# Performance work log

Hardware: AMD Instinct MI355X
Metric: run time of the kernel (lower is better)

The kernel has to match this reference:

```python
import jax, jax.numpy as jnp
import numpy as np

B, N, D = 8, 2048, 512

def setup_inputs() -> dict:
    key = jax.random.key(0)
    k1, k2, k3, k4, k5 = jax.random.split(key, 5)
    s = 1.0 / np.sqrt(D)
    return {
        "x": jax.random.normal(k1, (B, N, D), dtype=jnp.float32),
        "w_qkv": jax.random.normal(k2, (D, 3 * D), dtype=jnp.float32) * s,
        "b_qkv": jax.random.normal(k3, (3 * D,), dtype=jnp.float32) * 0.01,
        "w_fc": jax.random.normal(k4, (D, D), dtype=jnp.float32) * s,
        "b_fc": jax.random.normal(k5, (D,), dtype=jnp.float32) * 0.01,
    }

def reference(x, w_qkv, b_qkv, w_fc, b_fc):
    scale = 1.0 / (x.shape[-1] ** 0.5)
    qkv = x @ w_qkv + b_qkv                      # [B, N, 3D]
    q, k, v = jnp.split(qkv, 3, axis=-1)         # each [B, N, D]
    attn = jnp.einsum("bnd,bmd->bnm", q, k) * scale
    attn = jax.nn.softmax(attn, axis=-1)
    out = jnp.einsum("bnm,bmd->bnd", attn, v)
    return out @ w_fc + b_fc + x
```

## Files before the change

### kernel.cpp

```cpp
#include <hip/hip_runtime.h>
#include <stdint.h>

typedef unsigned short u16;
typedef unsigned int u32;
typedef __attribute__((ext_vector_type(8))) short short8;
typedef __attribute__((ext_vector_type(4))) float f32x4;
typedef __attribute__((ext_vector_type(8))) unsigned short u16x8;
typedef __attribute__((ext_vector_type(4))) float float4_t;

__device__ __forceinline__ float b2f(u16 u) { return __uint_as_float(((u32)u) << 16); }
__device__ __forceinline__ u16 f2b(float f) {
  u32 u = __float_as_uint(f);
  u += 0x7fffu + ((u >> 16) & 1u);
  return (u16)(u >> 16);
}

typedef const __attribute__((address_space(1))) void* gas_t;
typedef __attribute__((address_space(3))) void* las_t;
__device__ __forceinline__ void gl_lds16(const void* g, void* l) {
  __builtin_amdgcn_global_load_lds((gas_t)(uintptr_t)g, (las_t)(u32)(uintptr_t)l, 16, 0, 0);
}

__global__ __launch_bounds__(256) void cvt_f2b_kernel(const float* __restrict__ src,
                                                      u16* __restrict__ dst, long n) {
  long i = ((long)blockIdx.x * 256 + threadIdx.x) * 8;
  if (i >= n) return;
  float4_t v0 = *(const float4_t*)(src + i);
  float4_t v1 = *(const float4_t*)(src + i + 4);
  u16x8 o;
#pragma unroll
  for (int j = 0; j < 4; ++j) { o[j] = f2b(v0[j]); o[4 + j] = f2b(v1[j]); }
  *(u16x8*)(dst + i) = o;
}

__global__ __launch_bounds__(256) void tr_cvt(const float* __restrict__ src,
                                              u16* __restrict__ dst, int R, int C) {
  __shared__ float t[32][33];
  const int bx = blockIdx.x * 32;
  const int by = blockIdx.y * 32;
  const int tx = threadIdx.x & 31, ty = threadIdx.x >> 5;
#pragma unroll
  for (int i = 0; i < 32; i += 8)
    t[ty + i][tx] = src[(long)(by + ty + i) * C + bx + tx];
  __syncthreads();
#pragma unroll
  for (int i = 0; i < 32; i += 8)
    dst[(long)(bx + ty + i) * R + by + tx] = f2b(t[tx][ty + i]);
}

__global__ __launch_bounds__(256) void tr_v(const u16* __restrict__ qkv, u16* __restrict__ vt) {
  __shared__ u16 t[32][33];
  const int b = blockIdx.z;
  const int r0 = blockIdx.x * 32;
  const int d0 = blockIdx.y * 32;
  const int tx = threadIdx.x & 31, ty = threadIdx.x >> 5;
#pragma unroll
  for (int i = 0; i < 32; i += 8)
    t[ty + i][tx] = qkv[((long)b * 2048 + r0 + ty + i) * 1536 + 1024 + d0 + tx];
  __syncthreads();
#pragma unroll
  for (int i = 0; i < 32; i += 8)
    vt[((long)b * 512 + d0 + ty + i) * 2048 + r0 + tx] = t[tx][ty + i];
}

template <bool OUT_F32, bool BIAS, bool RES>
__global__ __launch_bounds__(256)
void gemm_bt(const u16* __restrict__ A, const u16* __restrict__ Bt, void* __restrict__ Cv,
             const float* __restrict__ bias, const float* __restrict__ res,
             int K, int lda, int ldb, int ldc,
             long aStride, long bStride, long cStride, float alpha) {
  __shared__ u16 As[2][128 * 32];
  __shared__ u16 Bs[2][128 * 32];
  const int tid = threadIdx.x;
  const int wid = tid >> 6, lane = tid & 63;
  const int wm = (wid >> 1) * 64, wn = (wid & 1) * 64;

  const int gx = gridDim.x, gy = gridDim.y;
  int id = (blockIdx.z * gy + blockIdx.y) * gx + blockIdx.x;
  const int nwg = gx * gy * gridDim.z;
  id = (id & 7) * (nwg >> 3) + (id >> 3);
  const int bxi = id % gx;
  const int t2 = id / gx;
  const int byi = t2 % gy;
  const long z = t2 / gy;

  A += z * aStride;
  Bt += z * bStride;
  const int by = byi * 128;
  const int bx = bxi * 128;

  f32x4 acc[4][4] = {};

  const int srow = wid * 32 + (lane >> 2);
  const int scol_lin = (lane & 3) * 8;
  const int scol_src = (((lane & 3) ^ ((lane >> 3) & 3)) * 8);
  const u16* Ag0 = A + (long)(by + srow) * lda + scol_src;
  const u16* Ag1 = Ag0 + (long)16 * lda;
  const u16* Bg0 = Bt + (long)(bx + srow) * ldb + scol_src;
  const u16* Bg1 = Bg0 + (long)16 * ldb;
  const int sL0 = srow * 32 + scol_lin;
  const int sL1 = sL0 + 16 * 32;
  const int lr = lane & 15, lg = lane >> 4;
  const int swz = ((lr >> 1) & 3) ^ lg;
  const int nK = K >> 5;

  auto stage = [&](int u, int nb) {
    const long ko = (long)u * 32;
    gl_lds16(Ag0 + ko, &As[nb][sL0]);
    gl_lds16(Ag1 + ko, &As[nb][sL1]);
    gl_lds16(Bg0 + ko, &Bs[nb][sL0]);
    gl_lds16(Bg1 + ko, &Bs[nb][sL1]);
  };

  stage(0, 0);

  for (int t = 0; t < nK; ++t) {
    const int cur = t & 1;
    asm volatile("s_waitcnt vmcnt(0)" ::: "memory");
    __builtin_amdgcn_s_barrier();
    __builtin_amdgcn_sched_barrier(0);
    if (t + 1 < nK) stage(t + 1, cur ^ 1);

    short8 a[4], b[4];
#pragma unroll
    for (int i = 0; i < 4; ++i) {
      a[i] = *(const short8*)&As[cur][(wm + i * 16 + lr) * 32 + swz * 8];
      b[i] = *(const short8*)&Bs[cur][(wn + i * 16 + lr) * 32 + swz * 8];
    }
    __builtin_amdgcn_s_setprio(1);
#pragma unroll
    for (int mi = 0; mi < 4; ++mi)
#pragma unroll
      for (int ni = 0; ni < 4; ++ni)
        acc[mi][ni] = __builtin_amdgcn_mfma_f32_16x16x32_bf16(a[mi], b[ni], acc[mi][ni], 0, 0, 0);
    __builtin_amdgcn_s_setprio(0);
  }

  if constexpr (OUT_F32) {
    float* C = (float*)Cv + z * cStride;
#pragma unroll
    for (int mi = 0; mi < 4; ++mi)
#pragma unroll
      for (int ni = 0; ni < 4; ++ni)
#pragma unroll
        for (int j = 0; j < 4; ++j) {
          const long row = by + wm + mi * 16 + lg * 4 + j;
          const int col = bx + wn + ni * 16 + lr;
          float v = acc[mi][ni][j] * alpha;
          if (BIAS) v += bias[col];
          if (RES) v += res[row * (long)ldc + col];
          C[row * (long)ldc + col] = v;
        }
  } else {
    u16* C = (u16*)Cv + z * cStride;
#pragma unroll
    for (int mi = 0; mi < 4; ++mi)
#pragma unroll
      for (int ni = 0; ni < 4; ++ni)
#pragma unroll
        for (int j = 0; j < 4; ++j) {
          const long row = by + wm + mi * 16 + lg * 4 + j;
          const int col = bx + wn + ni * 16 + lr;
          float v = acc[mi][ni][j] * alpha;
          if (BIAS) v += bias[col];
          C[row * (long)ldc + col] = f2b(v);
        }
  }
}

__global__ __launch_bounds__(256) void softmax_rows(u16* __restrict__ S) {
  const long row = blockIdx.x;
  u16* p = S + row * 2048;
  const int tid = threadIdx.x;
  const int wid = tid >> 6, lane = tid & 63;
  u16x8 v = ((const u16x8*)p)[tid];
  float f[8];
#pragma unroll
  for (int j = 0; j < 8; ++j) f[j] = b2f(v[j]);
  float m = f[0];
#pragma unroll
  for (int j = 1; j < 8; ++j) m = fmaxf(m, f[j]);
#pragma unroll
  for (int off = 32; off; off >>= 1) m = fmaxf(m, __shfl_xor(m, off));
  __shared__ float rmax[4], rsum[4];
  if (lane == 0) rmax[wid] = m;
  __syncthreads();
  m = fmaxf(fmaxf(rmax[0], rmax[1]), fmaxf(rmax[2], rmax[3]));
  float s = 0.f;
#pragma unroll
  for (int j = 0; j < 8; ++j) { f[j] = __expf(f[j] - m); s += f[j]; }
#pragma unroll
  for (int off = 32; off; off >>= 1) s += __shfl_xor(s, off);
  if (lane == 0) rsum[wid] = s;
  __syncthreads();
  s = rsum[0] + rsum[1] + rsum[2] + rsum[3];
  const float inv = 1.0f / s;
  u16x8 o;
#pragma unroll
  for (int j = 0; j < 8; ++j) o[j] = f2b(f[j] * inv);
  ((u16x8*)p)[tid] = o;
}

extern "C" void kernel_launch(void* const* d_in, const int* in_sizes, int n_in,
                              void* d_out, int out_size, void* d_ws, size_t ws_size,
                              hipStream_t stream) {
  const float* x = (const float*)d_in[0];
  const float* w_qkv = (const float*)d_in[1];
  const float* b_qkv = (const float*)d_in[2];
  const float* w_fc = (const float*)d_in[3];
  const float* b_fc = (const float*)d_in[4];
  float* out = (float*)d_out;

  char* ws = (char*)d_ws;
  const long MT = 16384;
  u16* xb = (u16*)(ws);
  u16* wqkvT = (u16*)(ws + 16777216);
  u16* wfcT = (u16*)(ws + 18350080);
  u16* qkv = (u16*)(ws + 18874368);
  u16* vt = (u16*)(ws + 69206016);
  u16* S = (u16*)(ws + 85983232);
  u16* attn = xb;

  cvt_f2b_kernel<<<4096, 256, 0, stream>>>(x, xb, MT * 512);
  tr_cvt<<<dim3(48, 16), 256, 0, stream>>>(w_qkv, wqkvT, 512, 1536);
  tr_cvt<<<dim3(16, 16), 256, 0, stream>>>(w_fc, wfcT, 512, 512);

  gemm_bt<false, true, false><<<dim3(12, 128, 1), 256, 0, stream>>>(
      xb, wqkvT, qkv, b_qkv, nullptr, 512, 512, 512, 1536, 0, 0, 0, 1.0f);

  tr_v<<<dim3(64, 16, 8), 256, 0, stream>>>(qkv, vt);

  gemm_bt<false, false, false><<<dim3(16, 16, 8), 256, 0, stream>>>(
      qkv, qkv + 512, S, nullptr, nullptr, 512, 1536, 1536, 2048,
      (long)2048 * 1536, (long)2048 * 1536, (long)2048 * 2048, 0.04419417382415922f);

  softmax_rows<<<16384, 256, 0, stream>>>(S);

  gemm_bt<false, false, false><<<dim3(4, 16, 8), 256, 0, stream>>>(
      S, vt, attn, nullptr, nullptr, 2048, 2048, 2048, 512,
      (long)2048 * 2048, (long)512 * 2048, (long)2048 * 512, 1.0f);

  gemm_bt<true, true, true><<<dim3(4, 128, 1), 256, 0, stream>>>(
      attn, wfcT, out, b_fc, x, 512, 512, 512, 512, 0, 0, 0, 1.0f);
}
```

Baseline: 190.9 us.

## Replace 128x128 GEMM with 256-row tiles, 512 threads and phased pipeline

Replaces the 128x128x32 bf16 GEMM with a 256xN (N=128 or 256) tile kernel using 8 waves, a 64-wide K step and a finer-grained schedule. Global-to-LDS loads for half-tiles are interleaved with four MFMA phases per buffer, separated by pinned barriers and partial vmcnt waits. Larger tiles increase operand reuse and cut global traffic per FLOP, and the phased staging aims to overlap loads with compute. In exchange it uses much more LDS (one block per CU) and gives fewer workgroups for the small GEMMs.

```diff
diff --git a/kernel.cpp b/kernel.cpp
--- a/kernel.cpp
+++ b/kernel.cpp
@@ -19,6 +19,11 @@
 typedef __attribute__((address_space(3))) void* las_t;
 __device__ __forceinline__ void gl_lds16(const void* g, void* l) {
   __builtin_amdgcn_global_load_lds((gas_t)(uintptr_t)g, (las_t)(u32)(uintptr_t)l, 16, 0, 0);
+}
+__device__ __forceinline__ void barrier_pin() {
+  __builtin_amdgcn_sched_barrier(0);
+  __builtin_amdgcn_s_barrier();
+  __builtin_amdgcn_sched_barrier(0);
 }
 
 __global__ __launch_bounds__(256) void cvt_f2b_kernel(const float* __restrict__ src,
@@ -63,17 +68,18 @@
     vt[((long)b * 512 + d0 + ty + i) * 2048 + r0 + tx] = t[tx][ty + i];
 }
 
-template <bool OUT_F32, bool BIAS, bool RES>
-__global__ __launch_bounds__(256)
-void gemm_bt(const u16* __restrict__ A, const u16* __restrict__ Bt, void* __restrict__ Cv,
+template <int NREP, bool OUT_F32, bool BIAS, bool RES>
+__global__ __launch_bounds__(512, 1)
+void gemm256(const u16* __restrict__ A, const u16* __restrict__ Bt, void* __restrict__ Cv,
              const float* __restrict__ bias, const float* __restrict__ res,
              int K, int lda, int ldb, int ldc,
              long aStride, long bStride, long cStride, float alpha) {
-  __shared__ u16 As[2][128 * 32];
-  __shared__ u16 Bs[2][128 * 32];
+  __shared__ u16 As[2][256 * 64];
+  __shared__ u16 Bs[2][NREP * 64 * 64];
   const int tid = threadIdx.x;
   const int wid = tid >> 6, lane = tid & 63;
-  const int wm = (wid >> 1) * 64, wn = (wid & 1) * 64;
+  const int wr = wid >> 2, wc = wid & 3;
+  const int lr = lane & 15, lg = lane >> 4;
 
   const int gx = gridDim.x, gy = gridDim.y;
   int id = (blockIdx.z * gy + blockIdx.y) * gx + blockIdx.x;
@@ -86,66 +92,132 @@
 
   A += z * aStride;
   Bt += z * bStride;
-  const int by = byi * 128;
-  const int bx = bxi * 128;
-
-  f32x4 acc[4][4] = {};
-
-  const int srow = wid * 32 + (lane >> 2);
-  const int scol_lin = (lane & 3) * 8;
-  const int scol_src = (((lane & 3) ^ ((lane >> 3) & 3)) * 8);
-  const u16* Ag0 = A + (long)(by + srow) * lda + scol_src;
-  const u16* Ag1 = Ag0 + (long)16 * lda;
-  const u16* Bg0 = Bt + (long)(bx + srow) * ldb + scol_src;
-  const u16* Bg1 = Bg0 + (long)16 * ldb;
-  const int sL0 = srow * 32 + scol_lin;
-  const int sL1 = sL0 + 16 * 32;
-  const int lr = lane & 15, lg = lane >> 4;
-  const int swz = ((lr >> 1) & 3) ^ lg;
-  const int nK = K >> 5;
-
-  auto stage = [&](int u, int nb) {
-    const long ko = (long)u * 32;
-    gl_lds16(Ag0 + ko, &As[nb][sL0]);
-    gl_lds16(Ag1 + ko, &As[nb][sL1]);
-    gl_lds16(Bg0 + ko, &Bs[nb][sL0]);
-    gl_lds16(Bg1 + ko, &Bs[nb][sL1]);
+  const int by = byi * 256;
+  const int bx = bxi * (NREP * 64);
+
+  f32x4 acc[8][NREP] = {};
+
+  const int w8l = wid * 8 + (lane >> 3);
+  const int scol_src = ((lane & 7) ^ (lane >> 3)) * 8;
+  const int scol_lin = (lane & 7) * 8;
+  const int nT = K >> 6;
+
+  auto stage_A = [&](int h, int kt) {
+    const int bb = kt & 1;
+    const long kc = (long)kt * 64 + scol_src;
+#pragma unroll
+    for (int r = 0; r < 2; ++r) {
+      const int row = h * 128 + r * 64 + w8l;
+      gl_lds16(A + (long)(by + row) * lda + kc, &As[bb][row * 64 + scol_lin]);
+    }
   };
-
-  stage(0, 0);
-
-  for (int t = 0; t < nK; ++t) {
-    const int cur = t & 1;
-    asm volatile("s_waitcnt vmcnt(0)" ::: "memory");
-    __builtin_amdgcn_s_barrier();
-    __builtin_amdgcn_sched_barrier(0);
-    if (t + 1 < nK) stage(t + 1, cur ^ 1);
-
-    short8 a[4], b[4];
-#pragma unroll
-    for (int i = 0; i < 4; ++i) {
-      a[i] = *(const short8*)&As[cur][(wm + i * 16 + lr) * 32 + swz * 8];
-      b[i] = *(const short8*)&Bs[cur][(wn + i * 16 + lr) * 32 + swz * 8];
+  auto stage_B = [&](int h, int kt) {
+    const int bb = kt & 1;
+    const long kc = (long)kt * 64 + scol_src;
+#pragma unroll
+    for (int r = 0; r < 2; ++r) {
+      const int row = h * 128 + r * 64 + w8l;
+      gl_lds16(Bt + (long)(bx + row) * ldb + kc, &Bs[bb][row * 64 + scol_lin]);
     }
-    __builtin_amdgcn_s_setprio(1);
-#pragma unroll
-    for (int mi = 0; mi < 4; ++mi)
-#pragma unroll
-      for (int ni = 0; ni < 4; ++ni)
-        acc[mi][ni] = __builtin_amdgcn_mfma_f32_16x16x32_bf16(a[mi], b[ni], acc[mi][ni], 0, 0, 0);
-    __builtin_amdgcn_s_setprio(0);
+  };
+
+  const int sx = lane & 7;
+  auto do_phase = [&](int bb, int q) {
+    if constexpr (NREP == 4) {
+      const int mh = q >> 1, nh = q & 1;
+      short8 a[4][2], b[2][2];
+#pragma unroll
+      for (int mi = 0; mi < 4; ++mi)
+#pragma unroll
+        for (int ks = 0; ks < 2; ++ks)
+          a[mi][ks] = *(const short8*)&As[bb][(mh * 128 + wr * 64 + mi * 16 + lr) * 64 +
+                                             (((ks * 4 + lg) ^ sx) * 8)];
+#pragma unroll
+      for (int ni = 0; ni < 2; ++ni)
+#pragma unroll
+        for (int ks = 0; ks < 2; ++ks)
+          b[ni][ks] = *(const short8*)&Bs[bb][(nh * 128 + wc * 32 + ni * 16 + lr) * 64 +
+                                             (((ks * 4 + lg) ^ sx) * 8)];
+      __builtin_amdgcn_s_setprio(1);
+#pragma unroll
+      for (int mi = 0; mi < 4; ++mi)
+#pragma unroll
+        for (int ni = 0; ni < 2; ++ni)
+#pragma unroll
+          for (int ks = 0; ks < 2; ++ks)
+            acc[mh * 4 + mi][nh * 2 + ni] = __builtin_amdgcn_mfma_f32_16x16x32_bf16(
+                a[mi][ks], b[ni][ks], acc[mh * 4 + mi][nh * 2 + ni], 0, 0, 0);
+      __builtin_amdgcn_s_setprio(0);
+    } else {
+      const int mh = q >> 1, kh = q & 1;
+      short8 a[4], b[2];
+#pragma unroll
+      for (int mi = 0; mi < 4; ++mi)
+        a[mi] = *(const short8*)&As[bb][(mh * 128 + wr * 64 + mi * 16 + lr) * 64 +
+                                        (((kh * 4 + lg) ^ sx) * 8)];
+#pragma unroll
+      for (int ni = 0; ni < 2; ++ni)
+        b[ni] = *(const short8*)&Bs[bb][(wc * 32 + ni * 16 + lr) * 64 +
+                                        (((kh * 4 + lg) ^ sx) * 8)];
+      __builtin_amdgcn_s_setprio(1);
+#pragma unroll
+      for (int mi = 0; mi < 4; ++mi)
+#pragma unroll
+        for (int ni = 0; ni < 2; ++ni)
+          acc[mh * 4 + mi][ni] = __builtin_amdgcn_mfma_f32_16x16x32_bf16(
+              a[mi], b[ni], acc[mh * 4 + mi][ni], 0, 0, 0);
+      __builtin_amdgcn_s_setprio(0);
+    }
+  };
+
+  stage_A(0, 0); stage_A(1, 0); stage_B(0, 0);
+  if constexpr (NREP == 4) stage_B(1, 0);
+  stage_A(0, 1);
+  asm volatile("s_waitcnt vmcnt(2)" ::: "memory");
+  barrier_pin();
+
+  for (int T = 0; T < nT; T += 2) {
+    const bool more = (T + 2) < nT;
+    stage_A(1, T + 1); stage_B(0, T + 1);
+    do_phase(0, 0);
+    barrier_pin();
+    if constexpr (NREP == 4) stage_B(1, T + 1);
+    do_phase(0, 1);
+    barrier_pin();
+    if (more) stage_A(0, T + 2);
+    do_phase(0, 2);
+    barrier_pin();
+    do_phase(0, 3);
+    if (more) asm volatile("s_waitcnt vmcnt(2)" ::: "memory");
+    else      asm volatile("s_waitcnt vmcnt(0)" ::: "memory");
+    barrier_pin();
+    if (more) stage_A(1, T + 2);
+    do_phase(1, 0);
+    barrier_pin();
+    if (more) stage_B(0, T + 2);
+    do_phase(1, 1);
+    barrier_pin();
+    if constexpr (NREP == 4) { if (more) stage_B(1, T + 2); }
+    do_phase(1, 2);
+    barrier_pin();
+    if (more) stage_A(0, T + 3);
+    do_phase(1, 3);
+    if (more) asm volatile("s_waitcnt vmcnt(2)" ::: "memory");
+    barrier_pin();
   }
 
   if constexpr (OUT_F32) {
     float* C = (float*)Cv + z * cStride;
 #pragma unroll
-    for (int mi = 0; mi < 4; ++mi)
-#pragma unroll
-      for (int ni = 0; ni < 4; ++ni)
+    for (int mi = 0; mi < 8; ++mi)
+#pragma unroll
+      for (int ni = 0; ni < NREP; ++ni)
 #pragma unroll
         for (int j = 0; j < 4; ++j) {
-          const long row = by + wm + mi * 16 + lg * 4 + j;
-          const int col = bx + wn + ni * 16 + lr;
+          const long row = by + (mi >> 2) * 128 + wr * 64 + (mi & 3) * 16 + lg * 4 + j;
+          const int col = (NREP == 4)
+                              ? bx + (ni >> 1) * 128 + wc * 32 + (ni & 1) * 16 + lr
+                              : bx + wc * 32 + ni * 16 + lr;
           float v = acc[mi][ni][j] * alpha;
           if (BIAS) v += bias[col];
           if (RES) v += res[row * (long)ldc + col];
@@ -154,13 +226,15 @@
   } else {
     u16* C = (u16*)Cv + z * cStride;
 #pragma unroll
-    for (int mi = 0; mi < 4; ++mi)
-#pragma unroll
-      for (int ni = 0; ni < 4; ++ni)
+    for (int mi = 0; mi < 8; ++mi)
+#pragma unroll
+      for (int ni = 0; ni < NREP; ++ni)
 #pragma unroll
         for (int j = 0; j < 4; ++j) {
-          const long row = by + wm + mi * 16 + lg * 4 + j;
-          const int col = bx + wn + ni * 16 + lr;
+          const long row = by + (mi >> 2) * 128 + wr * 64 + (mi & 3) * 16 + lg * 4 + j;
+          const int col = (NREP == 4)
+                              ? bx + (ni >> 1) * 128 + wc * 32 + (ni & 1) * 16 + lr
+                              : bx + wc * 32 + ni * 16 + lr;
           float v = acc[mi][ni][j] * alpha;
           if (BIAS) v += bias[col];
           C[row * (long)ldc + col] = f2b(v);
@@ -225,21 +299,21 @@
   tr_cvt<<<dim3(48, 16), 256, 0, stream>>>(w_qkv, wqkvT, 512, 1536);
   tr_cvt<<<dim3(16, 16), 256, 0, stream>>>(w_fc, wfcT, 512, 512);
 
-  gemm_bt<false, true, false><<<dim3(12, 128, 1), 256, 0, stream>>>(
+  gemm256<2, false, true, false><<<dim3(12, 64, 1), 512, 0, stream>>>(
       xb, wqkvT, qkv, b_qkv, nullptr, 512, 512, 512, 1536, 0, 0, 0, 1.0f);
 
   tr_v<<<dim3(64, 16, 8), 256, 0, stream>>>(qkv, vt);
 
-  gemm_bt<false, false, false><<<dim3(16, 16, 8), 256, 0, stream>>>(
+  gemm256<4, false, false, false><<<dim3(8, 8, 8), 512, 0, stream>>>(
       qkv, qkv + 512, S, nullptr, nullptr, 512, 1536, 1536, 2048,
       (long)2048 * 1536, (long)2048 * 1536, (long)2048 * 2048, 0.04419417382415922f);
 
   softmax_rows<<<16384, 256, 0, stream>>>(S);
 
-  gemm_bt<false, false, false><<<dim3(4, 16, 8), 256, 0, stream>>>(
+  gemm256<2, false, false, false><<<dim3(4, 8, 8), 512, 0, stream>>>(
       S, vt, attn, nullptr, nullptr, 2048, 2048, 2048, 512,
       (long)2048 * 2048, (long)512 * 2048, (long)2048 * 512, 1.0f);
 
-  gemm_bt<true, true, true><<<dim3(4, 128, 1), 256, 0, stream>>>(
+  gemm256<2, true, true, true><<<dim3(4, 64, 1), 512, 0, stream>>>(
       attn, wfcT, out, b_fc, x, 512, 512, 512, 512, 0, 0, 0, 1.0f);
 }
```

Result: no change. 189.1 us (-0.9%).
